# Kernel tuning notes

Measured on AMD Instinct MI355X. Metric: run time of the kernel, lower is better.

## Reference

```python
import jax, jax.numpy as jnp
import numpy as np

EPS_COS = 1e-8   # torch F.cosine_similarity eps
EPS_L1 = 1e-12   # torch F.normalize eps


def setup_inputs() -> dict:
    key = jax.random.key(0)
    k1, k2, k3, k4 = jax.random.split(key, 4)
    B, D, C = 32768, 768, 200
    features = jax.random.normal(k1, (B, D), dtype=jnp.float32)
    centers = jax.random.normal(k2, (C, D), dtype=jnp.float32)
    labels = jax.random.randint(k3, (B,), 0, C)
    labelled_or_not = jax.random.randint(k4, (B,), 0, 2).astype(jnp.bool_)
    return {"features": features, "centers": centers, "labels": labels,
            "labelled_or_not": labelled_or_not}


def reference(features, centers, labels, labelled_or_not):
    # cosine similarity: x.y / (max(|x|,eps) * max(|y|,eps))
    fn = features / jnp.maximum(jnp.linalg.norm(features, axis=1, keepdims=True), EPS_COS)
    cn = centers / jnp.maximum(jnp.linalg.norm(centers, axis=1, keepdims=True), EPS_COS)
    cos = jnp.einsum('bd,cd->bc', fn, cn)  # [B, C]

    # per-sample sign logic: label column -> +|cos|, all others -> -|cos|
    a = jnp.abs(cos)
    is_label = jax.nn.one_hot(labels, cos.shape[1], dtype=jnp.bool_)  # [B, C]
    signed = jnp.where(is_label, a, -a)

    # L1 normalize per row (||row||_1 == sum of |cos| regardless of signs)
    l1 = jnp.sum(a, axis=1, keepdims=True)
    normed = signed / jnp.maximum(l1, EPS_L1)

    # only labelled rows contribute (row-wise normalize is independent per row,
    # so masking after is equivalent to boolean-indexing before)
    contrib = jnp.where(labelled_or_not[:, None], normed, 0.0)
    return -jnp.sum(contrib)
```

## Files before the change

### kernel.cpp

```cpp
#include <hip/hip_runtime.h>
#include <hip/hip_bf16.h>

#define NROWS 32768
#define DIMS  768
#define NC    200
#define CPAD  256
#define KSTEP 32
#define NSTEP (DIMS / KSTEP)
#define ROWSB 64

typedef __attribute__((ext_vector_type(8))) short short8;
typedef __attribute__((ext_vector_type(4))) float f32x4;

__device__ __forceinline__ unsigned pk_bf16(float lo, float hi) {
  union { __hip_bfloat162 h; unsigned u; } c;
  c.h = __float22bfloat162_rn(make_float2(lo, hi));
  return c.u;
}

__global__ __launch_bounds__(256) void prep_centers_k(const float* __restrict__ centers,
                                                      short* __restrict__ cnb2,
                                                      float* __restrict__ out) {
  const int c = blockIdx.x;
  const int tid = threadIdx.x;
  if (c == 0 && tid == 0) out[0] = 0.f;
  if (c >= NC) {
    for (int d = tid; d < DIMS; d += 256)
      cnb2[(d >> 5) * (CPAD * KSTEP) + c * KSTEP + (d & 31)] = 0;
    return;
  }
  float ssq = 0.f;
  for (int d = tid; d < DIMS; d += 256) {
    float v = centers[c * DIMS + d];
    ssq += v * v;
  }
#pragma unroll
  for (int off = 32; off > 0; off >>= 1) ssq += __shfl_down(ssq, off);
  __shared__ float red[4];
  const int wid = tid >> 6, lane = tid & 63;
  if (lane == 0) red[wid] = ssq;
  __syncthreads();
  const float tot = red[0] + red[1] + red[2] + red[3];
  const float inv = 1.f / fmaxf(sqrtf(tot), 1e-8f);
  for (int d = tid; d < DIMS; d += 256) {
    const float v = centers[c * DIMS + d] * inv;
    union { __hip_bfloat16 h; short s; } cv;
    cv.h = __float2bfloat16(v);
    cnb2[(d >> 5) * (CPAD * KSTEP) + c * KSTEP + (d & 31)] = cv.s;
  }
}

__global__ __launch_bounds__(256) void cos_loss_k(
    const float* __restrict__ feats,
    const short* __restrict__ cnb2,
    const int* __restrict__ labels,
    const int* __restrict__ labelled,
    float* __restrict__ out) {
  const int tid = threadIdx.x;
  const int w = tid >> 6;
  const int lane = tid & 63;
  const int m = lane & 15;
  const int kg = lane >> 4;
  const int swzf = (m >> 1) & 3;
  const int rowBase = blockIdx.x * ROWSB;

  __shared__ short As[2][ROWSB][32];
  __shared__ short Bs[2][CPAD][32];
  __shared__ float invs[ROWSB];
  __shared__ int   labLds[ROWSB];
  __shared__ int   lblLds[ROWSB];
  __shared__ float l1part[4][ROWSB];
  __shared__ float alpart[4][ROWSB];

  if (tid < ROWSB) {
    labLds[tid] = labels[rowBase + tid];
    lblLds[tid] = labelled[rowBase + tid];
  }

  const int arow = tid >> 2;
  const int akg  = tid & 3;
  const int aswz = (arow >> 1) & 3;
  const float* asrc = feats + (size_t)(rowBase + arow) * DIMS + akg * 8;
  const int bcol = tid;
  const int bswz = (bcol >> 1) & 3;
  const short* bsrc = cnb2 + bcol * KSTEP;

  f32x4 acc[4][4];
#pragma unroll
  for (int mi = 0; mi < 4; ++mi)
#pragma unroll
    for (int ni = 0; ni < 4; ++ni) acc[mi][ni] = (f32x4){0.f, 0.f, 0.f, 0.f};

  float ssq = 0.f;

  float4 S0_alo, S0_ahi; short8 S0_b0, S0_b1, S0_b2, S0_b3;
  float4 S1_alo, S1_ahi; short8 S1_b0, S1_b1, S1_b2, S1_b3;

#define LOAD_SLOT(P, step) do {                                          \
    const float* ap_ = asrc + (step) * KSTEP;                            \
    P##_alo = *(const float4*)(ap_);                                     \
    P##_ahi = *(const float4*)(ap_ + 4);                                 \
    const short* bp_ = bsrc + (size_t)(step) * (CPAD * KSTEP);           \
    P##_b0 = *(const short8*)(bp_ + 0);                                  \
    P##_b1 = *(const short8*)(bp_ + 8);                                  \
    P##_b2 = *(const short8*)(bp_ + 16);                                 \
    P##_b3 = *(const short8*)(bp_ + 24);                                 \
  } while (0)

#define WRITE_SLOT(P, buf) do {                                          \
    ssq += P##_alo.x*P##_alo.x + P##_alo.y*P##_alo.y                     \
         + P##_alo.z*P##_alo.z + P##_alo.w*P##_alo.w;                    \
    ssq += P##_ahi.x*P##_ahi.x + P##_ahi.y*P##_ahi.y                     \
         + P##_ahi.z*P##_ahi.z + P##_ahi.w*P##_ahi.w;                    \
    union { short8 s; unsigned u[4]; } p_;                               \
    p_.u[0] = pk_bf16(P##_alo.x, P##_alo.y);                             \
    p_.u[1] = pk_bf16(P##_alo.z, P##_alo.w);                             \
    p_.u[2] = pk_bf16(P##_ahi.x, P##_ahi.y);                             \
    p_.u[3] = pk_bf16(P##_ahi.z, P##_ahi.w);                             \
    *(short8*)(&As[(buf)][arow][(akg ^ aswz) * 8]) = p_.s;               \
    *(short8*)(&Bs[(buf)][bcol][(0 ^ bswz) * 8]) = P##_b0;               \
    *(short8*)(&Bs[(buf)][bcol][(1 ^ bswz) * 8]) = P##_b1;               \
    *(short8*)(&Bs[(buf)][bcol][(2 ^ bswz) * 8]) = P##_b2;               \
    *(short8*)(&Bs[(buf)][bcol][(3 ^ bswz) * 8]) = P##_b3;               \
  } while (0)

#define COMPUTE(buf) do {                                                \
    short8 af[4], bf[4];                                                 \
    _Pragma("unroll")                                                    \
    for (int mi = 0; mi < 4; ++mi)                                       \
      af[mi] = *(const short8*)(&As[(buf)][mi * 16 + m][(kg ^ swzf) * 8]); \
    _Pragma("unroll")                                                    \
    for (int ni = 0; ni < 4; ++ni)                                       \
      bf[ni] = *(const short8*)(&Bs[(buf)][w * 64 + ni * 16 + m][(kg ^ swzf) * 8]); \
    _Pragma("unroll")                                                    \
    for (int mi = 0; mi < 4; ++mi)                                       \
      _Pragma("unroll")                                                  \
      for (int ni = 0; ni < 4; ++ni)                                     \
        acc[mi][ni] = __builtin_amdgcn_mfma_f32_16x16x32_bf16(           \
            af[mi], bf[ni], acc[mi][ni], 0, 0, 0);                       \
  } while (0)

  LOAD_SLOT(S0, 0);
  WRITE_SLOT(S0, 0);
  LOAD_SLOT(S1, 1);
  __syncthreads();

  for (int ks = 0; ks < NSTEP; ks += 2) {
    if (ks + 2 < NSTEP) LOAD_SLOT(S0, ks + 2);
    WRITE_SLOT(S1, 1);
    COMPUTE(0);
    __syncthreads();
    if (ks + 3 < NSTEP) LOAD_SLOT(S1, ks + 3);
    if (ks + 2 < NSTEP) WRITE_SLOT(S0, 0);
    COMPUTE(1);
    __syncthreads();
  }

#undef LOAD_SLOT
#undef WRITE_SLOT
#undef COMPUTE

  ssq += __shfl_xor(ssq, 1);
  ssq += __shfl_xor(ssq, 2);
  if ((tid & 3) == 0) invs[arow] = 1.f / fmaxf(sqrtf(ssq), 1e-8f);
  __syncthreads();

#pragma unroll
  for (int mi = 0; mi < 4; ++mi) {
    float l1r[4] = {0.f, 0.f, 0.f, 0.f};
    float alr[4] = {0.f, 0.f, 0.f, 0.f};
    float iv[4];
    int labr[4];
#pragma unroll
    for (int r = 0; r < 4; ++r) {
      const int row = mi * 16 + kg * 4 + r;
      iv[r] = invs[row];
      labr[r] = labLds[row];
    }
#pragma unroll
    for (int ni = 0; ni < 4; ++ni) {
      const int col = w * 64 + ni * 16 + m;
#pragma unroll
      for (int r = 0; r < 4; ++r) {
        const float a = fabsf(acc[mi][ni][r] * iv[r]);
        l1r[r] += a;
        if (col == labr[r]) alr[r] += a;
      }
    }
#pragma unroll
    for (int r = 0; r < 4; ++r) {
#pragma unroll
      for (int off = 1; off < 16; off <<= 1) {
        l1r[r] += __shfl_xor(l1r[r], off);
        alr[r] += __shfl_xor(alr[r], off);
      }
    }
    if (m == 0) {
#pragma unroll
      for (int r = 0; r < 4; ++r) {
        l1part[w][mi * 16 + kg * 4 + r] = l1r[r];
        alpart[w][mi * 16 + kg * 4 + r] = alr[r];
      }
    }
  }
  __syncthreads();

  if (tid < ROWSB) {
    const float L = l1part[0][tid] + l1part[1][tid] + l1part[2][tid] + l1part[3][tid];
    const float A = alpart[0][tid] + alpart[1][tid] + alpart[2][tid] + alpart[3][tid];
    float c = lblLds[tid] ? (L - 2.f * A) / fmaxf(L, 1e-12f) : 0.f;
#pragma unroll
    for (int off = 1; off < 64; off <<= 1) c += __shfl_xor(c, off);
    if (tid == 0) atomicAdd(out, c);
  }
}

extern "C" void kernel_launch(void* const* d_in, const int* in_sizes, int n_in,
                              void* d_out, int out_size, void* d_ws, size_t ws_size,
                              hipStream_t stream) {
  const float* feats = (const float*)d_in[0];
  const float* centers = (const float*)d_in[1];
  const int* labels = (const int*)d_in[2];
  const int* labelled = (const int*)d_in[3];
  float* out = (float*)d_out;
  short* cnb2 = (short*)d_ws;

  prep_centers_k<<<CPAD, 256, 0, stream>>>(centers, cnb2, out);
  cos_loss_k<<<NROWS / ROWSB, 256, 0, stream>>>(feats, cnb2, labels, labelled, out);
}
```

Measured before the change: 38.41 us.

## Halve rows per block and slim prefetch to raise occupancy

```diff
diff --git a/kernel.cpp b/kernel.cpp
--- a/kernel.cpp
+++ b/kernel.cpp
@@ -7,7 +7,7 @@
 #define CPAD  256
 #define KSTEP 32
 #define NSTEP (DIMS / KSTEP)
-#define ROWSB 64
+#define ROWSB 32
 
 typedef __attribute__((ext_vector_type(8))) short short8;
 typedef __attribute__((ext_vector_type(4))) float f32x4;
@@ -50,7 +50,7 @@
   }
 }
 
-__global__ __launch_bounds__(256) void cos_loss_k(
+__global__ __launch_bounds__(256, 4) void cos_loss_k(
     const float* __restrict__ feats,
     const short* __restrict__ cnb2,
     const int* __restrict__ labels,
@@ -77,96 +77,93 @@
     lblLds[tid] = labelled[rowBase + tid];
   }
 
-  const int arow = tid >> 2;
-  const int akg  = tid & 3;
+  const int arow = tid >> 3;
+  const int ac   = tid & 7;
+  const int aq   = ac >> 1;
+  const int ah   = ac & 1;
   const int aswz = (arow >> 1) & 3;
-  const float* asrc = feats + (size_t)(rowBase + arow) * DIMS + akg * 8;
+  const float* asrc = feats + (size_t)(rowBase + arow) * DIMS + ac * 4;
+  short* adst0 = &As[0][arow][(aq ^ aswz) * 8 + ah * 4];
+  short* adst1 = &As[1][arow][(aq ^ aswz) * 8 + ah * 4];
   const int bcol = tid;
   const int bswz = (bcol >> 1) & 3;
   const short* bsrc = cnb2 + bcol * KSTEP;
 
-  f32x4 acc[4][4];
-#pragma unroll
-  for (int mi = 0; mi < 4; ++mi)
+  f32x4 acc[2][4];
+#pragma unroll
+  for (int mi = 0; mi < 2; ++mi)
 #pragma unroll
     for (int ni = 0; ni < 4; ++ni) acc[mi][ni] = (f32x4){0.f, 0.f, 0.f, 0.f};
 
   float ssq = 0.f;
-
-  float4 S0_alo, S0_ahi; short8 S0_b0, S0_b1, S0_b2, S0_b3;
-  float4 S1_alo, S1_ahi; short8 S1_b0, S1_b1, S1_b2, S1_b3;
-
-#define LOAD_SLOT(P, step) do {                                          \
-    const float* ap_ = asrc + (step) * KSTEP;                            \
-    P##_alo = *(const float4*)(ap_);                                     \
-    P##_ahi = *(const float4*)(ap_ + 4);                                 \
+  float4 pva;
+  short8 pb0, pb1, pb2, pb3;
+
+#define LOAD_STEP(step) do {                                             \
+    pva = *(const float4*)(asrc + (step) * KSTEP);                       \
     const short* bp_ = bsrc + (size_t)(step) * (CPAD * KSTEP);           \
-    P##_b0 = *(const short8*)(bp_ + 0);                                  \
-    P##_b1 = *(const short8*)(bp_ + 8);                                  \
-    P##_b2 = *(const short8*)(bp_ + 16);                                 \
-    P##_b3 = *(const short8*)(bp_ + 24);                                 \
+    pb0 = *(const short8*)(bp_ + 0);                                     \
+    pb1 = *(const short8*)(bp_ + 8);                                     \
+    pb2 = *(const short8*)(bp_ + 16);                                    \
+    pb3 = *(const short8*)(bp_ + 24);                                    \
   } while (0)
 
-#define WRITE_SLOT(P, buf) do {                                          \
-    ssq += P##_alo.x*P##_alo.x + P##_alo.y*P##_alo.y                     \
-         + P##_alo.z*P##_alo.z + P##_alo.w*P##_alo.w;                    \
-    ssq += P##_ahi.x*P##_ahi.x + P##_ahi.y*P##_ahi.y                     \
-         + P##_ahi.z*P##_ahi.z + P##_ahi.w*P##_ahi.w;                    \
-    union { short8 s; unsigned u[4]; } p_;                               \
-    p_.u[0] = pk_bf16(P##_alo.x, P##_alo.y);                             \
-    p_.u[1] = pk_bf16(P##_alo.z, P##_alo.w);                             \
-    p_.u[2] = pk_bf16(P##_ahi.x, P##_ahi.y);                             \
-    p_.u[3] = pk_bf16(P##_ahi.z, P##_ahi.w);                             \
-    *(short8*)(&As[(buf)][arow][(akg ^ aswz) * 8]) = p_.s;               \
-    *(short8*)(&Bs[(buf)][bcol][(0 ^ bswz) * 8]) = P##_b0;               \
-    *(short8*)(&Bs[(buf)][bcol][(1 ^ bswz) * 8]) = P##_b1;               \
-    *(short8*)(&Bs[(buf)][bcol][(2 ^ bswz) * 8]) = P##_b2;               \
-    *(short8*)(&Bs[(buf)][bcol][(3 ^ bswz) * 8]) = P##_b3;               \
+#define WRITE_STEP(adst, buf) do {                                       \
+    ssq += pva.x*pva.x + pva.y*pva.y + pva.z*pva.z + pva.w*pva.w;        \
+    union { unsigned u[2]; } p_;                                         \
+    p_.u[0] = pk_bf16(pva.x, pva.y);                                     \
+    p_.u[1] = pk_bf16(pva.z, pva.w);                                     \
+    *(unsigned*)(adst) = p_.u[0];                                        \
+    *(unsigned*)((adst) + 2) = p_.u[1];                                  \
+    *(short8*)(&Bs[(buf)][bcol][(0 ^ bswz) * 8]) = pb0;                  \
+    *(short8*)(&Bs[(buf)][bcol][(1 ^ bswz) * 8]) = pb1;                  \
+    *(short8*)(&Bs[(buf)][bcol][(2 ^ bswz) * 8]) = pb2;                  \
+    *(short8*)(&Bs[(buf)][bcol][(3 ^ bswz) * 8]) = pb3;                  \
   } while (0)
 
 #define COMPUTE(buf) do {                                                \
-    short8 af[4], bf[4];                                                 \
-    _Pragma("unroll")                                                    \
-    for (int mi = 0; mi < 4; ++mi)                                       \
-      af[mi] = *(const short8*)(&As[(buf)][mi * 16 + m][(kg ^ swzf) * 8]); \
+    short8 af0, af1, bf[4];                                              \
+    af0 = *(const short8*)(&As[(buf)][m][(kg ^ swzf) * 8]);              \
+    af1 = *(const short8*)(&As[(buf)][16 + m][(kg ^ swzf) * 8]);         \
     _Pragma("unroll")                                                    \
     for (int ni = 0; ni < 4; ++ni)                                       \
       bf[ni] = *(const short8*)(&Bs[(buf)][w * 64 + ni * 16 + m][(kg ^ swzf) * 8]); \
     _Pragma("unroll")                                                    \
-    for (int mi = 0; mi < 4; ++mi)                                       \
-      _Pragma("unroll")                                                  \
-      for (int ni = 0; ni < 4; ++ni)                                     \
-        acc[mi][ni] = __builtin_amdgcn_mfma_f32_16x16x32_bf16(           \
-            af[mi], bf[ni], acc[mi][ni], 0, 0, 0);                       \
+    for (int ni = 0; ni < 4; ++ni) {                                     \
+      acc[0][ni] = __builtin_amdgcn_mfma_f32_16x16x32_bf16(af0, bf[ni], acc[0][ni], 0, 0, 0); \
+      acc[1][ni] = __builtin_amdgcn_mfma_f32_16x16x32_bf16(af1, bf[ni], acc[1][ni], 0, 0, 0); \
+    }                                                                    \
   } while (0)
 
-  LOAD_SLOT(S0, 0);
-  WRITE_SLOT(S0, 0);
-  LOAD_SLOT(S1, 1);
+  LOAD_STEP(0);
+  WRITE_STEP(adst0, 0);
   __syncthreads();
 
   for (int ks = 0; ks < NSTEP; ks += 2) {
-    if (ks + 2 < NSTEP) LOAD_SLOT(S0, ks + 2);
-    WRITE_SLOT(S1, 1);
+    if (ks + 1 < NSTEP) LOAD_STEP(ks + 1);
     COMPUTE(0);
+    if (ks + 1 < NSTEP) WRITE_STEP(adst1, 1);
     __syncthreads();
-    if (ks + 3 < NSTEP) LOAD_SLOT(S1, ks + 3);
-    if (ks + 2 < NSTEP) WRITE_SLOT(S0, 0);
-    COMPUTE(1);
-    __syncthreads();
-  }
-
-#undef LOAD_SLOT
-#undef WRITE_SLOT
+    if (ks + 1 < NSTEP) {
+      if (ks + 2 < NSTEP) LOAD_STEP(ks + 2);
+      COMPUTE(1);
+      if (ks + 2 < NSTEP) WRITE_STEP(adst0, 0);
+      __syncthreads();
+    }
+  }
+
+#undef LOAD_STEP
+#undef WRITE_STEP
 #undef COMPUTE
 
   ssq += __shfl_xor(ssq, 1);
   ssq += __shfl_xor(ssq, 2);
-  if ((tid & 3) == 0) invs[arow] = 1.f / fmaxf(sqrtf(ssq), 1e-8f);
-  __syncthreads();
-
-#pragma unroll
-  for (int mi = 0; mi < 4; ++mi) {
+  ssq += __shfl_xor(ssq, 4);
+  if (ac == 0) invs[arow] = 1.f / fmaxf(sqrtf(ssq), 1e-8f);
+  __syncthreads();
+
+#pragma unroll
+  for (int mi = 0; mi < 2; ++mi) {
     float l1r[4] = {0.f, 0.f, 0.f, 0.f};
     float alr[4] = {0.f, 0.f, 0.f, 0.f};
     float iv[4];
@@ -210,7 +207,7 @@
     const float A = alpart[0][tid] + alpart[1][tid] + alpart[2][tid] + alpart[3][tid];
     float c = lblLds[tid] ? (L - 2.f * A) / fmaxf(L, 1e-12f) : 0.f;
 #pragma unroll
-    for (int off = 1; off < 64; off <<= 1) c += __shfl_xor(c, off);
+    for (int off = 1; off < 32; off <<= 1) c += __shfl_xor(c, off);
     if (tid == 0) atomicAdd(out, c);
   }
 }
```

Result: slower. 50.51 us (+31.5%).

## Load pre-swizzled center tiles directly into LDS via global_load_lds

Applied to the files above, without the earlier changes.

```diff
diff --git a/kernel.cpp b/kernel.cpp
--- a/kernel.cpp
+++ b/kernel.cpp
@@ -18,15 +18,22 @@
   return c.u;
 }
 
+__device__ __forceinline__ void glds16(const void* g, void* l) {
+  __builtin_amdgcn_global_load_lds(
+      (const __attribute__((address_space(1))) unsigned int*)g,
+      (__attribute__((address_space(3))) unsigned int*)l, 16, 0, 0);
+}
+
 __global__ __launch_bounds__(256) void prep_centers_k(const float* __restrict__ centers,
                                                       short* __restrict__ cnb2,
                                                       float* __restrict__ out) {
   const int c = blockIdx.x;
   const int tid = threadIdx.x;
   if (c == 0 && tid == 0) out[0] = 0.f;
+  const int cswz = (c >> 1) & 3;
   if (c >= NC) {
     for (int d = tid; d < DIMS; d += 256)
-      cnb2[(d >> 5) * (CPAD * KSTEP) + c * KSTEP + (d & 31)] = 0;
+      cnb2[(d >> 5) * (CPAD * KSTEP) + c * KSTEP + d % 32] = 0;
     return;
   }
   float ssq = 0.f;
@@ -46,7 +53,8 @@
     const float v = centers[c * DIMS + d] * inv;
     union { __hip_bfloat16 h; short s; } cv;
     cv.h = __float2bfloat16(v);
-    cnb2[(d >> 5) * (CPAD * KSTEP) + c * KSTEP + (d & 31)] = cv.s;
+    const int ks = d >> 5, dk = d & 31, q = dk >> 3, j = dk & 7;
+    cnb2[ks * (CPAD * KSTEP) + c * KSTEP + ((q ^ cswz) * 8 + j)] = cv.s;
   }
 }
 
@@ -61,7 +69,7 @@
   const int lane = tid & 63;
   const int m = lane & 15;
   const int kg = lane >> 4;
-  const int swzf = (m >> 1) & 3;
+  const int sq = (kg ^ ((m >> 1) & 3)) * 8;
   const int rowBase = blockIdx.x * ROWSB;
 
   __shared__ short As[2][ROWSB][32];
@@ -78,12 +86,11 @@
   }
 
   const int arow = tid >> 2;
-  const int akg  = tid & 3;
+  const int aq   = tid & 3;
   const int aswz = (arow >> 1) & 3;
-  const float* asrc = feats + (size_t)(rowBase + arow) * DIMS + akg * 8;
-  const int bcol = tid;
-  const int bswz = (bcol >> 1) & 3;
-  const short* bsrc = cnb2 + bcol * KSTEP;
+  const float* asrc = feats + (size_t)(rowBase + arow) * DIMS + aq * 8;
+  short* adst[2] = { &As[0][arow][(aq ^ aswz) * 8], &As[1][arow][(aq ^ aswz) * 8] };
+  const short* bbase = cnb2 + (size_t)(w * 64) * KSTEP + lane * 8;
 
   f32x4 acc[4][4];
 #pragma unroll
@@ -92,46 +99,43 @@
     for (int ni = 0; ni < 4; ++ni) acc[mi][ni] = (f32x4){0.f, 0.f, 0.f, 0.f};
 
   float ssq = 0.f;
-
-  float4 S0_alo, S0_ahi; short8 S0_b0, S0_b1, S0_b2, S0_b3;
-  float4 S1_alo, S1_ahi; short8 S1_b0, S1_b1, S1_b2, S1_b3;
-
-#define LOAD_SLOT(P, step) do {                                          \
+  float4 S0_lo, S0_hi, S1_lo, S1_hi;
+
+#define LOADA(P, step) do {                                              \
     const float* ap_ = asrc + (step) * KSTEP;                            \
-    P##_alo = *(const float4*)(ap_);                                     \
-    P##_ahi = *(const float4*)(ap_ + 4);                                 \
-    const short* bp_ = bsrc + (size_t)(step) * (CPAD * KSTEP);           \
-    P##_b0 = *(const short8*)(bp_ + 0);                                  \
-    P##_b1 = *(const short8*)(bp_ + 8);                                  \
-    P##_b2 = *(const short8*)(bp_ + 16);                                 \
-    P##_b3 = *(const short8*)(bp_ + 24);                                 \
-  } while (0)
-
-#define WRITE_SLOT(P, buf) do {                                          \
-    ssq += P##_alo.x*P##_alo.x + P##_alo.y*P##_alo.y                     \
-         + P##_alo.z*P##_alo.z + P##_alo.w*P##_alo.w;                    \
-    ssq += P##_ahi.x*P##_ahi.x + P##_ahi.y*P##_ahi.y                     \
-         + P##_ahi.z*P##_ahi.z + P##_ahi.w*P##_ahi.w;                    \
+    P##_lo = *(const float4*)(ap_);                                      \
+    P##_hi = *(const float4*)(ap_ + 4);                                  \
+  } while (0)
+
+#define WRITEA(P, buf) do {                                              \
+    ssq += P##_lo.x*P##_lo.x + P##_lo.y*P##_lo.y                         \
+         + P##_lo.z*P##_lo.z + P##_lo.w*P##_lo.w;                        \
+    ssq += P##_hi.x*P##_hi.x + P##_hi.y*P##_hi.y                         \
+         + P##_hi.z*P##_hi.z + P##_hi.w*P##_hi.w;                        \
     union { short8 s; unsigned u[4]; } p_;                               \
-    p_.u[0] = pk_bf16(P##_alo.x, P##_alo.y);                             \
-    p_.u[1] = pk_bf16(P##_alo.z, P##_alo.w);                             \
-    p_.u[2] = pk_bf16(P##_ahi.x, P##_ahi.y);                             \
-    p_.u[3] = pk_bf16(P##_ahi.z, P##_ahi.w);                             \
-    *(short8*)(&As[(buf)][arow][(akg ^ aswz) * 8]) = p_.s;               \
-    *(short8*)(&Bs[(buf)][bcol][(0 ^ bswz) * 8]) = P##_b0;               \
-    *(short8*)(&Bs[(buf)][bcol][(1 ^ bswz) * 8]) = P##_b1;               \
-    *(short8*)(&Bs[(buf)][bcol][(2 ^ bswz) * 8]) = P##_b2;               \
-    *(short8*)(&Bs[(buf)][bcol][(3 ^ bswz) * 8]) = P##_b3;               \
+    p_.u[0] = pk_bf16(P##_lo.x, P##_lo.y);                               \
+    p_.u[1] = pk_bf16(P##_lo.z, P##_lo.w);                               \
+    p_.u[2] = pk_bf16(P##_hi.x, P##_hi.y);                               \
+    p_.u[3] = pk_bf16(P##_hi.z, P##_hi.w);                               \
+    *(short8*)(adst[(buf)]) = p_.s;                                      \
+  } while (0)
+
+#define DMAB(step, buf) do {                                             \
+    const short* g_ = bbase + (size_t)(step) * (CPAD * KSTEP);           \
+    glds16(g_ + 0 * (16 * KSTEP), &Bs[(buf)][w * 64 + 0 * 16][0]);       \
+    glds16(g_ + 1 * (16 * KSTEP), &Bs[(buf)][w * 64 + 1 * 16][0]);       \
+    glds16(g_ + 2 * (16 * KSTEP), &Bs[(buf)][w * 64 + 2 * 16][0]);       \
+    glds16(g_ + 3 * (16 * KSTEP), &Bs[(buf)][w * 64 + 3 * 16][0]);       \
   } while (0)
 
 #define COMPUTE(buf) do {                                                \
     short8 af[4], bf[4];                                                 \
     _Pragma("unroll")                                                    \
     for (int mi = 0; mi < 4; ++mi)                                       \
-      af[mi] = *(const short8*)(&As[(buf)][mi * 16 + m][(kg ^ swzf) * 8]); \
+      af[mi] = *(const short8*)(&As[(buf)][mi * 16 + m][sq]);            \
     _Pragma("unroll")                                                    \
     for (int ni = 0; ni < 4; ++ni)                                       \
-      bf[ni] = *(const short8*)(&Bs[(buf)][w * 64 + ni * 16 + m][(kg ^ swzf) * 8]); \
+      bf[ni] = *(const short8*)(&Bs[(buf)][w * 64 + ni * 16 + m][sq]);   \
     _Pragma("unroll")                                                    \
     for (int mi = 0; mi < 4; ++mi)                                       \
       _Pragma("unroll")                                                  \
@@ -140,24 +144,30 @@
             af[mi], bf[ni], acc[mi][ni], 0, 0, 0);                       \
   } while (0)
 
-  LOAD_SLOT(S0, 0);
-  WRITE_SLOT(S0, 0);
-  LOAD_SLOT(S1, 1);
+  LOADA(S0, 0);
+  LOADA(S1, 1);
+  DMAB(0, 0);
+  WRITEA(S0, 0);
   __syncthreads();
 
   for (int ks = 0; ks < NSTEP; ks += 2) {
-    if (ks + 2 < NSTEP) LOAD_SLOT(S0, ks + 2);
-    WRITE_SLOT(S1, 1);
+    DMAB(ks + 1, 1);
+    if (ks + 2 < NSTEP) LOADA(S0, ks + 2);
+    WRITEA(S1, 1);
     COMPUTE(0);
     __syncthreads();
-    if (ks + 3 < NSTEP) LOAD_SLOT(S1, ks + 3);
-    if (ks + 2 < NSTEP) WRITE_SLOT(S0, 0);
+    if (ks + 2 < NSTEP) {
+      DMAB(ks + 2, 0);
+      if (ks + 3 < NSTEP) LOADA(S1, ks + 3);
+      WRITEA(S0, 0);
+    }
     COMPUTE(1);
     __syncthreads();
   }
 
-#undef LOAD_SLOT
-#undef WRITE_SLOT
+#undef LOADA
+#undef WRITEA
+#undef DMAB
 #undef COMPUTE
 
   ssq += __shfl_xor(ssq, 1);
```

Measured after the change: 38.41 us. About the same (-0.0%).
